# Optimization experiments

Measured on AMD Instinct MI355X. Metric: run time of the kernel, lower is better.

The kernel has to match this reference:

```python
import jax, jax.numpy as jnp
import numpy as np

HEADS = 12


def setup_inputs() -> dict:
    key = jax.random.key(0)
    ks = jax.random.split(key, 3)
    B, N, C = 4, 2048, 768
    x = jax.random.normal(ks[0], (B, N, C), dtype=jnp.float32)
    Wqkv = jax.random.normal(ks[1], (C, 3 * C), dtype=jnp.float32) * 0.02
    bqkv = jnp.zeros((3 * C,), dtype=jnp.float32)
    Wproj = jax.random.normal(ks[2], (C, C), dtype=jnp.float32) * 0.02
    bproj = jnp.zeros((C,), dtype=jnp.float32)
    return {"x": x, "Wqkv": Wqkv, "bqkv": bqkv, "Wproj": Wproj, "bproj": bproj}


def reference(x, Wqkv, bqkv, Wproj, bproj):
    B, N, C = x.shape
    h = HEADS
    d = C // h
    scale = d ** (-0.5)
    # QKV projection: (B, N, 3C) -> (3, B, h, N, d)
    qkv = (x @ Wqkv + bqkv).reshape(B, N, 3, h, d).transpose(2, 0, 3, 1, 4)
    q, k, v = qkv[0], qkv[1], qkv[2]
    # Full N x N attention scores per head (matches original explicit matmul)
    scores = jnp.einsum("bhnd,bhmd->bhnm", q, k) * scale
    attn = jax.nn.softmax(scores, axis=-1)
    out = jnp.einsum("bhnm,bhmd->bhnd", attn, v)  # (B, h, N, d)
    out = out.transpose(0, 2, 1, 3).reshape(B, N, C)
    return out @ Wproj + bproj
```

## Files before the change

kernel.cpp:

```cpp
#include <hip/hip_runtime.h>
#include <hip/hip_bf16.h>
#include <math.h>

#define B_ 4
#define N_ 2048
#define C_ 768
#define H_ 12
#define D_ 64
#define SC_LOG2E 0.18033688f

typedef __attribute__((ext_vector_type(8))) short bf16x8;
typedef __attribute__((ext_vector_type(4))) float f32x4;

#define MFMA16(A, B, C) __builtin_amdgcn_mfma_f32_16x16x32_bf16(A, B, C, 0, 0, 0)

#if __has_builtin(__builtin_amdgcn_exp2f)
#define EXP2F(x) __builtin_amdgcn_exp2f(x)
#else
#define EXP2F(x) exp2f(x)
#endif

__device__ __forceinline__ ushort f2bf(float f) {
    union { float f; unsigned u; } v; v.f = f;
    unsigned r = v.u + 0x7fffu + ((v.u >> 16) & 1u);
    return (ushort)(r >> 16);
}

#if __has_builtin(__builtin_amdgcn_cvt_pk_bf16_f32)
typedef __attribute__((ext_vector_type(2))) __bf16 bf16x2v;
__device__ __forceinline__ unsigned pack_bf2(float a, float b) {
    union { bf16x2v v; unsigned u; } cv;
    cv.v = __builtin_amdgcn_cvt_pk_bf16_f32(a, b);
    return cv.u;
}
#else
__device__ __forceinline__ unsigned pack_bf2(float a, float b) {
    union { __hip_bfloat162 h2; unsigned u; } cv;
    cv.h2 = __float22bfloat162_rn(make_float2(a, b));
    return cv.u;
}
#endif

__device__ __forceinline__ void gl_lds16(const ushort* g, ushort* l) {
    __builtin_amdgcn_global_load_lds(
        (const __attribute__((address_space(1))) unsigned*)g,
        (__attribute__((address_space(3))) unsigned*)l, 16, 0, 0);
}

__device__ __forceinline__ void tr_body(const float* __restrict__ W,
                                        ushort* __restrict__ Wt,
                                        int K, int N, int bx, int by, int t) {
    __shared__ float T[32][33];
    int k0 = by * 32, n0 = bx * 32;
    int r = t >> 3, c4 = (t & 7) * 4;
    float4 v = *(const float4*)&W[(size_t)(k0 + r) * N + n0 + c4];
    T[r][c4] = v.x; T[r][c4 + 1] = v.y; T[r][c4 + 2] = v.z; T[r][c4 + 3] = v.w;
    __syncthreads();
    union { ushort s[4]; unsigned long long u; } o;
    o.s[0] = f2bf(T[c4 + 0][r]);
    o.s[1] = f2bf(T[c4 + 1][r]);
    o.s[2] = f2bf(T[c4 + 2][r]);
    o.s[3] = f2bf(T[c4 + 3][r]);
    *(unsigned long long*)&Wt[(size_t)(n0 + r) * K + k0 + c4] = o.u;
}

__global__ __launch_bounds__(256) void prep(
    const float* __restrict__ x, ushort* __restrict__ xb,
    const float* __restrict__ Wqkv, ushort* __restrict__ Wqkvt,
    const float* __restrict__ Wproj, ushort* __restrict__ Wprojt)
{
    const int bid = blockIdx.x, t = threadIdx.x;
    if (bid < 3072) {
        int i = bid * 256 + t;
        const float4* p = (const float4*)x + 2 * (size_t)i;
        float4 a = p[0], bq = p[1];
        union { ushort s[8]; uint4 v; } u;
        u.s[0] = f2bf(a.x);  u.s[1] = f2bf(a.y);  u.s[2] = f2bf(a.z);  u.s[3] = f2bf(a.w);
        u.s[4] = f2bf(bq.x); u.s[5] = f2bf(bq.y); u.s[6] = f2bf(bq.z); u.s[7] = f2bf(bq.w);
        *(uint4*)&xb[(size_t)i * 8] = u.v;
    } else if (bid < 4800) {
        int id = bid - 3072;
        tr_body(Wqkv, Wqkvt, C_, 3 * C_, id % 72, id / 72, t);
    } else {
        int id = bid - 4800;
        tr_body(Wproj, Wprojt, C_, C_, id % 24, id / 24, t);
    }
}

__global__ __launch_bounds__(256) void vtrans(const ushort* __restrict__ qkvb,
                                              ushort* __restrict__ Vt) {
    __shared__ ushort T[64 * 64];
    const int tid = threadIdx.x;
    const int t0 = blockIdx.x * 64, bh = blockIdx.y;
    const int b = bh / H_, h = bh % H_;
#pragma unroll
    for (int i = 0; i < 2; i++) {
        int c = i * 256 + tid;
        int tok = c >> 3, dc = c & 7;
        uint4 v = *(const uint4*)&qkvb[((size_t)b * N_ + t0 + tok) * (3 * C_)
                                       + 2 * C_ + h * D_ + dc * 8];
        const ushort* vs = (const ushort*)&v;
#pragma unroll
        for (int j = 0; j < 8; j++) {
            int d = dc * 8 + j;
            int sc = (tok >> 3) ^ (d & 7) ^ (d >> 3);
            T[d * 64 + sc * 8 + (tok & 7)] = vs[j];
        }
    }
    __syncthreads();
#pragma unroll
    for (int i = 0; i < 2; i++) {
        int c = i * 256 + tid;
        int d = c >> 3, tc = c & 7;
        int sc = tc ^ (d & 7) ^ (d >> 3);
        uint4 o = *(const uint4*)&T[d * 64 + sc * 8];
        *(uint4*)&Vt[((size_t)bh * D_ + d) * N_ + t0 + tc * 8] = o;
    }
}

template <bool OBF>
__global__ __launch_bounds__(256) void gemm_bf16(
    const ushort* __restrict__ A, const ushort* __restrict__ Bt,
    const float* __restrict__ bias, void* __restrict__ outp,
    int M, int N, int K)
{
    __shared__ ushort Asl[128 * 64];
    __shared__ ushort Bsl[128 * 64];

    const int tid  = threadIdx.x;
    const int lane = tid & 63, w = tid >> 6;
    const int quad = lane >> 4, l16 = lane & 15;
    const int row0 = blockIdx.y * 128, col0 = blockIdx.x * 128;
    const int mh = (w >> 1) * 64, nh = (w & 1) * 64;

    f32x4 acc[4][4];
#pragma unroll
    for (int i = 0; i < 4; i++)
#pragma unroll
        for (int j = 0; j < 4; j++) acc[i][j] = (f32x4)0.f;

    for (int k0 = 0; k0 < K; k0 += 64) {
#pragma unroll
        for (int i = 0; i < 4; i++) {
            int c  = i * 256 + w * 64 + lane;
            int rr = c >> 3;
            int cc = (c & 7) ^ (rr & 7);
            int wb = (i * 256 + w * 64) * 8;
            gl_lds16(&A[(size_t)(row0 + rr) * K + k0 + cc * 8], &Asl[wb]);
            gl_lds16(&Bt[(size_t)(col0 + rr) * K + k0 + cc * 8], &Bsl[wb]);
        }
        __syncthreads();
#pragma unroll
        for (int h = 0; h < 2; h++) {
            const int sw = ((h * 4 + quad) ^ (l16 & 7)) * 8;
            bf16x8 af[4], bfr[4];
#pragma unroll
            for (int mt = 0; mt < 4; mt++)
                af[mt] = *(const bf16x8*)&Asl[(mh + mt * 16 + l16) * 64 + sw];
#pragma unroll
            for (int nt = 0; nt < 4; nt++)
                bfr[nt] = *(const bf16x8*)&Bsl[(nh + nt * 16 + l16) * 64 + sw];
#pragma unroll
            for (int mt = 0; mt < 4; mt++)
#pragma unroll
                for (int nt = 0; nt < 4; nt++)
                    acc[mt][nt] = MFMA16(af[mt], bfr[nt], acc[mt][nt]);
        }
        __syncthreads();
    }

    const float scl = (OBF && col0 < C_) ? SC_LOG2E : 1.f;
#pragma unroll
    for (int nt = 0; nt < 4; nt++) {
        int col = col0 + nh + nt * 16 + l16;
        float bv = bias[col];
#pragma unroll
        for (int mt = 0; mt < 4; mt++) {
            f32x4 v = acc[mt][nt];
#pragma unroll
            for (int r = 0; r < 4; r++) {
                int row = row0 + mh + mt * 16 + quad * 4 + r;
                if (OBF)
                    ((ushort*)outp)[(size_t)row * N + col] = f2bf((v[r] + bv) * scl);
                else
                    ((float*)outp)[(size_t)row * N + col] = v[r] + bv;
            }
        }
    }
}

__global__ __launch_bounds__(256) void attn_mfma(
    const ushort* __restrict__ qkvb, const ushort* __restrict__ Vt,
    ushort* __restrict__ attnb)
{
    __shared__ ushort Kd[3][64 * 64];
    __shared__ ushort Vd[3][64 * 64];
    __shared__ ushort Ptl[4 * 32 * 72];

    const int tid  = threadIdx.x;
    const int lane = tid & 63, w = tid >> 6;
    const int quad = lane >> 4, l16 = lane & 15;

    const int flat = blockIdx.y * 16 + blockIdx.x;
    const int nf   = (flat & 7) * 96 + (flat >> 3);
    const int bh   = nf >> 4, qt_ = nf & 15;
    const int b = bh / H_, h = bh % H_;
    const int q0 = qt_ * 128 + w * 32;
    const size_t rowbase = (size_t)b * N_;
    const int hoff = h * D_;
    ushort* Ptw = Ptl + w * 32 * 72;
    const f32x4 Z4 = {0.f, 0.f, 0.f, 0.f};

    const ushort* Kg = qkvb + rowbase * (3 * C_) + C_ + hoff;
    const ushort* Vg = Vt + (size_t)bh * D_ * N_;

    int rr0, cc0, rr1, cc1, wb0, wb1;
    {
        int c0 = w * 64 + lane, c1 = 256 + w * 64 + lane;
        rr0 = c0 >> 3; cc0 = (c0 & 7) ^ (rr0 & 7); wb0 = (w * 64) * 8;
        rr1 = c1 >> 3; cc1 = (c1 & 7) ^ (rr1 & 7); wb1 = (256 + w * 64) * 8;
    }
    const ushort* kp0 = Kg + (size_t)rr0 * (3 * C_) + cc0 * 8;
    const ushort* kp1 = Kg + (size_t)rr1 * (3 * C_) + cc1 * 8;
    const ushort* vp0 = Vg + (size_t)rr0 * N_ + cc0 * 8;
    const ushort* vp1 = Vg + (size_t)rr1 * N_ + cc1 * 8;

    bf16x8 Qf[2][2];
#pragma unroll
    for (int qt = 0; qt < 2; qt++)
#pragma unroll
        for (int c = 0; c < 2; c++)
            Qf[qt][c] = *(const bf16x8*)&qkvb[(rowbase + q0 + qt * 16 + l16) * (3 * C_)
                                              + hoff + c * 32 + quad * 8];

    f32x4 oacc[4][2];
#pragma unroll
    for (int dt = 0; dt < 4; dt++)
#pragma unroll
        for (int qt = 0; qt < 2; qt++) oacc[dt][qt] = (f32x4)0.f;
    float lrow[2] = {0.f, 0.f};

    const int NT = N_ / 64;
    gl_lds16(kp0, &Kd[0][wb0]); gl_lds16(vp0, &Vd[0][wb0]);
    gl_lds16(kp1, &Kd[0][wb1]); gl_lds16(vp1, &Vd[0][wb1]);
    kp0 += (size_t)64 * 3 * C_; kp1 += (size_t)64 * 3 * C_; vp0 += 64; vp1 += 64;
    gl_lds16(kp0, &Kd[1][wb0]); gl_lds16(vp0, &Vd[1][wb0]);
    gl_lds16(kp1, &Kd[1][wb1]); gl_lds16(vp1, &Vd[1][wb1]);
    kp0 += (size_t)64 * 3 * C_; kp1 += (size_t)64 * 3 * C_; vp0 += 64; vp1 += 64;
    asm volatile("s_waitcnt vmcnt(4)" ::: "memory");
    __builtin_amdgcn_s_barrier();
    __builtin_amdgcn_sched_barrier(0);

    int rd = 0;
    for (int t = 0; t < NT; ++t) {
        int wr = rd + 2; if (wr >= 3) wr -= 3;
        if (t + 2 < NT) {
            gl_lds16(kp0, &Kd[wr][wb0]); gl_lds16(vp0, &Vd[wr][wb0]);
            gl_lds16(kp1, &Kd[wr][wb1]); gl_lds16(vp1, &Vd[wr][wb1]);
            kp0 += (size_t)64 * 3 * C_; kp1 += (size_t)64 * 3 * C_;
            vp0 += 64; vp1 += 64;
        }
        __builtin_amdgcn_sched_barrier(0);

        const ushort* Kb = Kd[rd];
        const ushort* Vb = Vd[rd];

        f32x4 sacc[4][2];
        {
            bf16x8 kf[4];
#pragma unroll
            for (int kt = 0; kt < 4; kt++)
                kf[kt] = *(const bf16x8*)&Kb[(kt * 16 + l16) * 64
                                             + ((quad) ^ (l16 & 7)) * 8];
            __builtin_amdgcn_s_setprio(1);
#pragma unroll
            for (int kt = 0; kt < 4; kt++)
#pragma unroll
                for (int qt = 0; qt < 2; qt++)
                    sacc[kt][qt] = MFMA16(kf[kt], Qf[qt][0], Z4);
            __builtin_amdgcn_s_setprio(0);
        }
        {
            bf16x8 kf[4];
#pragma unroll
            for (int kt = 0; kt < 4; kt++)
                kf[kt] = *(const bf16x8*)&Kb[(kt * 16 + l16) * 64
                                             + ((4 | quad) ^ (l16 & 7)) * 8];
            __builtin_amdgcn_s_setprio(1);
#pragma unroll
            for (int kt = 0; kt < 4; kt++)
#pragma unroll
                for (int qt = 0; qt < 2; qt++)
                    sacc[kt][qt] = MFMA16(kf[kt], Qf[qt][1], sacc[kt][qt]);
            __builtin_amdgcn_s_setprio(0);
        }

#pragma unroll
        for (int qt = 0; qt < 2; qt++) {
            float sum = 0.f;
#pragma unroll
            for (int kt = 0; kt < 4; kt++) {
                float p0 = EXP2F(sacc[kt][qt][0]);
                float p1 = EXP2F(sacc[kt][qt][1]);
                float p2 = EXP2F(sacc[kt][qt][2]);
                float p3 = EXP2F(sacc[kt][qt][3]);
                sum += (p0 + p1) + (p2 + p3);
                uint2 pk;
                pk.x = pack_bf2(p0, p1);
                pk.y = pack_bf2(p2, p3);
                *(uint2*)&Ptw[(qt * 16 + l16) * 72 + kt * 16 + quad * 4] = pk;
            }
            lrow[qt] += sum;
        }

#pragma unroll
        for (int c = 0; c < 2; c++) {
            bf16x8 pf[2];
#pragma unroll
            for (int qt = 0; qt < 2; qt++)
                pf[qt] = *(const bf16x8*)&Ptw[(qt * 16 + l16) * 72
                                              + c * 32 + quad * 8];
            __builtin_amdgcn_s_setprio(1);
#pragma unroll
            for (int dt = 0; dt < 4; dt++) {
                bf16x8 vf = *(const bf16x8*)&Vb[(dt * 16 + l16) * 64
                                   + (((c << 2) | quad) ^ (l16 & 7)) * 8];
#pragma unroll
                for (int qt = 0; qt < 2; qt++)
                    oacc[dt][qt] = MFMA16(vf, pf[qt], oacc[dt][qt]);
            }
            __builtin_amdgcn_s_setprio(0);
        }

        if (t < NT - 2) asm volatile("s_waitcnt vmcnt(4)" ::: "memory");
        else            asm volatile("s_waitcnt vmcnt(0)" ::: "memory");
        __builtin_amdgcn_s_barrier();
        __builtin_amdgcn_sched_barrier(0);
        rd++; if (rd == 3) rd = 0;
    }

#pragma unroll
    for (int qt = 0; qt < 2; qt++) {
        float s = lrow[qt];
        s += __shfl_xor(s, 16, 64);
        s += __shfl_xor(s, 32, 64);
        float inv = 1.f / s;
        size_t orow = (rowbase + q0 + qt * 16 + l16) * C_ + hoff;
#pragma unroll
        for (int dt = 0; dt < 4; dt++) {
            union { ushort us[4]; unsigned long long u; } o;
#pragma unroll
            for (int r = 0; r < 4; r++) o.us[r] = f2bf(oacc[dt][qt][r] * inv);
            *(unsigned long long*)&attnb[orow + dt * 16 + quad * 4] = o.u;
        }
    }
}

extern "C" void kernel_launch(void* const* d_in, const int* in_sizes, int n_in,
                              void* d_out, int out_size, void* d_ws, size_t ws_size,
                              hipStream_t stream)
{
    const float* x     = (const float*)d_in[0];
    const float* Wqkv  = (const float*)d_in[1];
    const float* bqkv  = (const float*)d_in[2];
    const float* Wproj = (const float*)d_in[3];
    const float* bproj = (const float*)d_in[4];

    ushort* xb     = (ushort*)d_ws;
    ushort* Wqkvt  = xb + (size_t)B_ * N_ * C_;
    ushort* Wprojt = Wqkvt + (size_t)3 * C_ * C_;
    ushort* qkvb   = Wprojt + (size_t)C_ * C_;
    ushort* attnb  = qkvb + (size_t)B_ * N_ * 3 * C_;
    ushort* Vtb    = attnb + (size_t)B_ * N_ * C_;

    const int M = B_ * N_;

    prep<<<5376, 256, 0, stream>>>(x, xb, Wqkv, Wqkvt, Wproj, Wprojt);

    gemm_bf16<true><<<dim3((3 * C_) / 128, M / 128), 256, 0, stream>>>(
        xb, Wqkvt, bqkv, qkvb, M, 3 * C_, C_);

    vtrans<<<dim3(N_ / 64, B_ * H_), 256, 0, stream>>>(qkvb, Vtb);

    attn_mfma<<<dim3(N_ / 128, B_ * H_), 256, 0, stream>>>(qkvb, Vtb, attnb);

    gemm_bf16<false><<<dim3(C_ / 128, M / 128), 256, 0, stream>>>(
        attnb, Wprojt, bproj, d_out, M, C_, C_);
}
```

Before: 250.9 us.

## Fuse V transpose into QKV GEMM epilogue and use 8-wave attention blocks

The QKV GEMM epilogue now writes the V columns straight into the head-major transposed layout, so the separate vtrans kernel and its extra pass over V are gone. The attention kernel moves from 4 waves with 32 query rows each to 8 waves with 16 rows each. It also drops from triple to double buffering of K/V tiles with one load per thread, and sets launch bounds to 512 threads. This is meant to raise occupancy and cut register pressure. In exchange each K/V tile is reused across fewer query rows per wave, and a full vmcnt(0) wait every iteration reduces prefetch depth.

```diff
diff --git a/kernel.cpp b/kernel.cpp
--- a/kernel.cpp
+++ b/kernel.cpp
@@ -87,41 +87,11 @@
     }
 }
 
-__global__ __launch_bounds__(256) void vtrans(const ushort* __restrict__ qkvb,
-                                              ushort* __restrict__ Vt) {
-    __shared__ ushort T[64 * 64];
-    const int tid = threadIdx.x;
-    const int t0 = blockIdx.x * 64, bh = blockIdx.y;
-    const int b = bh / H_, h = bh % H_;
-#pragma unroll
-    for (int i = 0; i < 2; i++) {
-        int c = i * 256 + tid;
-        int tok = c >> 3, dc = c & 7;
-        uint4 v = *(const uint4*)&qkvb[((size_t)b * N_ + t0 + tok) * (3 * C_)
-                                       + 2 * C_ + h * D_ + dc * 8];
-        const ushort* vs = (const ushort*)&v;
-#pragma unroll
-        for (int j = 0; j < 8; j++) {
-            int d = dc * 8 + j;
-            int sc = (tok >> 3) ^ (d & 7) ^ (d >> 3);
-            T[d * 64 + sc * 8 + (tok & 7)] = vs[j];
-        }
-    }
-    __syncthreads();
-#pragma unroll
-    for (int i = 0; i < 2; i++) {
-        int c = i * 256 + tid;
-        int d = c >> 3, tc = c & 7;
-        int sc = tc ^ (d & 7) ^ (d >> 3);
-        uint4 o = *(const uint4*)&T[d * 64 + sc * 8];
-        *(uint4*)&Vt[((size_t)bh * D_ + d) * N_ + t0 + tc * 8] = o;
-    }
-}
-
 template <bool OBF>
 __global__ __launch_bounds__(256) void gemm_bf16(
     const ushort* __restrict__ A, const ushort* __restrict__ Bt,
     const float* __restrict__ bias, void* __restrict__ outp,
+    ushort* __restrict__ vtp,
     int M, int N, int K)
 {
     __shared__ ushort Asl[128 * 64];
@@ -169,33 +139,52 @@
         __syncthreads();
     }
 
-    const float scl = (OBF && col0 < C_) ? SC_LOG2E : 1.f;
-#pragma unroll
-    for (int nt = 0; nt < 4; nt++) {
-        int col = col0 + nh + nt * 16 + l16;
-        float bv = bias[col];
-#pragma unroll
-        for (int mt = 0; mt < 4; mt++) {
-            f32x4 v = acc[mt][nt];
-#pragma unroll
-            for (int r = 0; r < 4; r++) {
-                int row = row0 + mh + mt * 16 + quad * 4 + r;
-                if (OBF)
-                    ((ushort*)outp)[(size_t)row * N + col] = f2bf((v[r] + bv) * scl);
-                else
-                    ((float*)outp)[(size_t)row * N + col] = v[r] + bv;
+    if (OBF && col0 >= 2 * C_) {
+#pragma unroll
+        for (int nt = 0; nt < 4; nt++) {
+            int colh = col0 - 2 * C_ + nh + nt * 16 + l16;
+            int hh = colh >> 6, dd = colh & 63;
+            float bv = bias[col0 + nh + nt * 16 + l16];
+#pragma unroll
+            for (int mt = 0; mt < 4; mt++) {
+                f32x4 v = acc[mt][nt];
+                int row = row0 + mh + mt * 16 + quad * 4;
+                int bb = row >> 11, tok = row & (N_ - 1);
+                union { ushort us[4]; unsigned long long u; } o;
+#pragma unroll
+                for (int r = 0; r < 4; r++) o.us[r] = f2bf(v[r] + bv);
+                *(unsigned long long*)&vtp[((size_t)(bb * H_ + hh) * D_ + dd) * N_ + tok] = o.u;
             }
         }
-    }
-}
-
-__global__ __launch_bounds__(256) void attn_mfma(
+    } else {
+        const float scl = (OBF && col0 < C_) ? SC_LOG2E : 1.f;
+#pragma unroll
+        for (int nt = 0; nt < 4; nt++) {
+            int col = col0 + nh + nt * 16 + l16;
+            float bv = bias[col];
+#pragma unroll
+            for (int mt = 0; mt < 4; mt++) {
+                f32x4 v = acc[mt][nt];
+#pragma unroll
+                for (int r = 0; r < 4; r++) {
+                    int row = row0 + mh + mt * 16 + quad * 4 + r;
+                    if (OBF)
+                        ((ushort*)outp)[(size_t)row * N + col] = f2bf((v[r] + bv) * scl);
+                    else
+                        ((float*)outp)[(size_t)row * N + col] = v[r] + bv;
+                }
+            }
+        }
+    }
+}
+
+__global__ __launch_bounds__(512, 6) void attn_mfma(
     const ushort* __restrict__ qkvb, const ushort* __restrict__ Vt,
     ushort* __restrict__ attnb)
 {
-    __shared__ ushort Kd[3][64 * 64];
-    __shared__ ushort Vd[3][64 * 64];
-    __shared__ ushort Ptl[4 * 32 * 72];
+    __shared__ ushort Kd[2][64 * 64];
+    __shared__ ushort Vd[2][64 * 64];
+    __shared__ ushort Ptl[8 * 16 * 72];
 
     const int tid  = threadIdx.x;
     const int lane = tid & 63, w = tid >> 6;
@@ -205,67 +194,53 @@
     const int nf   = (flat & 7) * 96 + (flat >> 3);
     const int bh   = nf >> 4, qt_ = nf & 15;
     const int b = bh / H_, h = bh % H_;
-    const int q0 = qt_ * 128 + w * 32;
+    const int q0 = qt_ * 128 + w * 16;
     const size_t rowbase = (size_t)b * N_;
     const int hoff = h * D_;
-    ushort* Ptw = Ptl + w * 32 * 72;
+    ushort* Ptw = Ptl + w * 16 * 72;
     const f32x4 Z4 = {0.f, 0.f, 0.f, 0.f};
 
     const ushort* Kg = qkvb + rowbase * (3 * C_) + C_ + hoff;
     const ushort* Vg = Vt + (size_t)bh * D_ * N_;
 
-    int rr0, cc0, rr1, cc1, wb0, wb1;
-    {
-        int c0 = w * 64 + lane, c1 = 256 + w * 64 + lane;
-        rr0 = c0 >> 3; cc0 = (c0 & 7) ^ (rr0 & 7); wb0 = (w * 64) * 8;
-        rr1 = c1 >> 3; cc1 = (c1 & 7) ^ (rr1 & 7); wb1 = (256 + w * 64) * 8;
-    }
-    const ushort* kp0 = Kg + (size_t)rr0 * (3 * C_) + cc0 * 8;
-    const ushort* kp1 = Kg + (size_t)rr1 * (3 * C_) + cc1 * 8;
-    const ushort* vp0 = Vg + (size_t)rr0 * N_ + cc0 * 8;
-    const ushort* vp1 = Vg + (size_t)rr1 * N_ + cc1 * 8;
-
-    bf16x8 Qf[2][2];
-#pragma unroll
-    for (int qt = 0; qt < 2; qt++)
-#pragma unroll
-        for (int c = 0; c < 2; c++)
-            Qf[qt][c] = *(const bf16x8*)&qkvb[(rowbase + q0 + qt * 16 + l16) * (3 * C_)
-                                              + hoff + c * 32 + quad * 8];
-
-    f32x4 oacc[4][2];
-#pragma unroll
-    for (int dt = 0; dt < 4; dt++)
-#pragma unroll
-        for (int qt = 0; qt < 2; qt++) oacc[dt][qt] = (f32x4)0.f;
-    float lrow[2] = {0.f, 0.f};
+    const int rr = tid >> 3;
+    const int cc = (tid & 7) ^ (rr & 7);
+    const int wbase = w * 512;
+    const ushort* kp = Kg + (size_t)rr * (3 * C_) + cc * 8;
+    const ushort* vp = Vg + (size_t)rr * N_ + cc * 8;
+
+    bf16x8 Qf[2];
+#pragma unroll
+    for (int c = 0; c < 2; c++)
+        Qf[c] = *(const bf16x8*)&qkvb[(rowbase + q0 + l16) * (3 * C_)
+                                      + hoff + c * 32 + quad * 8];
+
+    f32x4 oacc[4];
+#pragma unroll
+    for (int dt = 0; dt < 4; dt++) oacc[dt] = (f32x4)0.f;
+    float lrow = 0.f;
 
     const int NT = N_ / 64;
-    gl_lds16(kp0, &Kd[0][wb0]); gl_lds16(vp0, &Vd[0][wb0]);
-    gl_lds16(kp1, &Kd[0][wb1]); gl_lds16(vp1, &Vd[0][wb1]);
-    kp0 += (size_t)64 * 3 * C_; kp1 += (size_t)64 * 3 * C_; vp0 += 64; vp1 += 64;
-    gl_lds16(kp0, &Kd[1][wb0]); gl_lds16(vp0, &Vd[1][wb0]);
-    gl_lds16(kp1, &Kd[1][wb1]); gl_lds16(vp1, &Vd[1][wb1]);
-    kp0 += (size_t)64 * 3 * C_; kp1 += (size_t)64 * 3 * C_; vp0 += 64; vp1 += 64;
-    asm volatile("s_waitcnt vmcnt(4)" ::: "memory");
+    gl_lds16(kp, &Kd[0][wbase]);
+    gl_lds16(vp, &Vd[0][wbase]);
+    kp += (size_t)64 * 3 * C_; vp += 64;
+    asm volatile("s_waitcnt vmcnt(0)" ::: "memory");
     __builtin_amdgcn_s_barrier();
     __builtin_amdgcn_sched_barrier(0);
 
-    int rd = 0;
     for (int t = 0; t < NT; ++t) {
-        int wr = rd + 2; if (wr >= 3) wr -= 3;
-        if (t + 2 < NT) {
-            gl_lds16(kp0, &Kd[wr][wb0]); gl_lds16(vp0, &Vd[wr][wb0]);
-            gl_lds16(kp1, &Kd[wr][wb1]); gl_lds16(vp1, &Vd[wr][wb1]);
-            kp0 += (size_t)64 * 3 * C_; kp1 += (size_t)64 * 3 * C_;
-            vp0 += 64; vp1 += 64;
+        const int rd = t & 1, wr = rd ^ 1;
+        if (t + 1 < NT) {
+            gl_lds16(kp, &Kd[wr][wbase]);
+            gl_lds16(vp, &Vd[wr][wbase]);
+            kp += (size_t)64 * 3 * C_; vp += 64;
         }
         __builtin_amdgcn_sched_barrier(0);
 
         const ushort* Kb = Kd[rd];
         const ushort* Vb = Vd[rd];
 
-        f32x4 sacc[4][2];
+        f32x4 sacc[4];
         {
             bf16x8 kf[4];
 #pragma unroll
@@ -275,9 +250,7 @@
             __builtin_amdgcn_s_setprio(1);
 #pragma unroll
             for (int kt = 0; kt < 4; kt++)
-#pragma unroll
-                for (int qt = 0; qt < 2; qt++)
-                    sacc[kt][qt] = MFMA16(kf[kt], Qf[qt][0], Z4);
+                sacc[kt] = MFMA16(kf[kt], Qf[0], Z4);
             __builtin_amdgcn_s_setprio(0);
         }
         {
@@ -289,68 +262,56 @@
             __builtin_amdgcn_s_setprio(1);
 #pragma unroll
             for (int kt = 0; kt < 4; kt++)
-#pragma unroll
-                for (int qt = 0; qt < 2; qt++)
-                    sacc[kt][qt] = MFMA16(kf[kt], Qf[qt][1], sacc[kt][qt]);
+                sacc[kt] = MFMA16(kf[kt], Qf[1], sacc[kt]);
             __builtin_amdgcn_s_setprio(0);
         }
 
-#pragma unroll
-        for (int qt = 0; qt < 2; qt++) {
+        {
             float sum = 0.f;
 #pragma unroll
             for (int kt = 0; kt < 4; kt++) {
-                float p0 = EXP2F(sacc[kt][qt][0]);
-                float p1 = EXP2F(sacc[kt][qt][1]);
-                float p2 = EXP2F(sacc[kt][qt][2]);
-                float p3 = EXP2F(sacc[kt][qt][3]);
+                float p0 = EXP2F(sacc[kt][0]);
+                float p1 = EXP2F(sacc[kt][1]);
+                float p2 = EXP2F(sacc[kt][2]);
+                float p3 = EXP2F(sacc[kt][3]);
                 sum += (p0 + p1) + (p2 + p3);
                 uint2 pk;
                 pk.x = pack_bf2(p0, p1);
                 pk.y = pack_bf2(p2, p3);
-                *(uint2*)&Ptw[(qt * 16 + l16) * 72 + kt * 16 + quad * 4] = pk;
+                *(uint2*)&Ptw[l16 * 72 + kt * 16 + quad * 4] = pk;
             }
-            lrow[qt] += sum;
+            lrow += sum;
         }
 
 #pragma unroll
         for (int c = 0; c < 2; c++) {
-            bf16x8 pf[2];
-#pragma unroll
-            for (int qt = 0; qt < 2; qt++)
-                pf[qt] = *(const bf16x8*)&Ptw[(qt * 16 + l16) * 72
-                                              + c * 32 + quad * 8];
+            bf16x8 pf = *(const bf16x8*)&Ptw[l16 * 72 + c * 32 + quad * 8];
             __builtin_amdgcn_s_setprio(1);
 #pragma unroll
             for (int dt = 0; dt < 4; dt++) {
                 bf16x8 vf = *(const bf16x8*)&Vb[(dt * 16 + l16) * 64
                                    + (((c << 2) | quad) ^ (l16 & 7)) * 8];
-#pragma unroll
-                for (int qt = 0; qt < 2; qt++)
-                    oacc[dt][qt] = MFMA16(vf, pf[qt], oacc[dt][qt]);
+                oacc[dt] = MFMA16(vf, pf, oacc[dt]);
             }
             __builtin_amdgcn_s_setprio(0);
         }
 
-        if (t < NT - 2) asm volatile("s_waitcnt vmcnt(4)" ::: "memory");
-        else            asm volatile("s_waitcnt vmcnt(0)" ::: "memory");
+        asm volatile("s_waitcnt vmcnt(0)" ::: "memory");
         __builtin_amdgcn_s_barrier();
         __builtin_amdgcn_sched_barrier(0);
-        rd++; if (rd == 3) rd = 0;
-    }
-
-#pragma unroll
-    for (int qt = 0; qt < 2; qt++) {
-        float s = lrow[qt];
+    }
+
+    {
+        float s = lrow;
         s += __shfl_xor(s, 16, 64);
         s += __shfl_xor(s, 32, 64);
         float inv = 1.f / s;
-        size_t orow = (rowbase + q0 + qt * 16 + l16) * C_ + hoff;
+        size_t orow = (rowbase + q0 + l16) * C_ + hoff;
 #pragma unroll
         for (int dt = 0; dt < 4; dt++) {
             union { ushort us[4]; unsigned long long u; } o;
 #pragma unroll
-            for (int r = 0; r < 4; r++) o.us[r] = f2bf(oacc[dt][qt][r] * inv);
+            for (int r = 0; r < 4; r++) o.us[r] = f2bf(oacc[dt][r] * inv);
             *(unsigned long long*)&attnb[orow + dt * 16 + quad * 4] = o.u;
         }
     }
@@ -378,12 +339,10 @@
     prep<<<5376, 256, 0, stream>>>(x, xb, Wqkv, Wqkvt, Wproj, Wprojt);
 
     gemm_bf16<true><<<dim3((3 * C_) / 128, M / 128), 256, 0, stream>>>(
-        xb, Wqkvt, bqkv, qkvb, M, 3 * C_, C_);
-
-    vtrans<<<dim3(N_ / 64, B_ * H_), 256, 0, stream>>>(qkvb, Vtb);
-
-    attn_mfma<<<dim3(N_ / 128, B_ * H_), 256, 0, stream>>>(qkvb, Vtb, attnb);
+        xb, Wqkvt, bqkv, qkvb, Vtb, M, 3 * C_, C_);
+
+    attn_mfma<<<dim3(N_ / 128, B_ * H_), 512, 0, stream>>>(qkvb, Vtb, attnb);
 
     gemm_bf16<false><<<dim3(C_ / 128, M / 128), 256, 0, stream>>>(
-        attnb, Wprojt, bproj, d_out, M, C_, C_);
-}
+        attnb, Wprojt, bproj, d_out, nullptr, M, C_, C_);
+}
```

Result: faster. 225.4 us (-10.2%).

## Fuse V transpose into QKV GEMM epilogue and double-buffer attention K/V

Applied to the files above, without the earlier changes.

The QKV GEMM epilogue now writes the V columns straight into the head-major transposed Vt layout, packing four consecutive tokens per 8-byte store. This removes the separate vtrans kernel launch and its read and write of V. The attention kernel also drops from a triple-buffered to a double-buffered K/V pipeline with full vmcnt(0) waits each iteration. That cuts LDS use, which may allow more blocks per CU, but it reduces how far loads run ahead of compute and so exposes more load latency.

```diff
diff --git a/kernel.cpp b/kernel.cpp
--- a/kernel.cpp
+++ b/kernel.cpp
@@ -87,41 +87,11 @@
     }
 }
 
-__global__ __launch_bounds__(256) void vtrans(const ushort* __restrict__ qkvb,
-                                              ushort* __restrict__ Vt) {
-    __shared__ ushort T[64 * 64];
-    const int tid = threadIdx.x;
-    const int t0 = blockIdx.x * 64, bh = blockIdx.y;
-    const int b = bh / H_, h = bh % H_;
-#pragma unroll
-    for (int i = 0; i < 2; i++) {
-        int c = i * 256 + tid;
-        int tok = c >> 3, dc = c & 7;
-        uint4 v = *(const uint4*)&qkvb[((size_t)b * N_ + t0 + tok) * (3 * C_)
-                                       + 2 * C_ + h * D_ + dc * 8];
-        const ushort* vs = (const ushort*)&v;
-#pragma unroll
-        for (int j = 0; j < 8; j++) {
-            int d = dc * 8 + j;
-            int sc = (tok >> 3) ^ (d & 7) ^ (d >> 3);
-            T[d * 64 + sc * 8 + (tok & 7)] = vs[j];
-        }
-    }
-    __syncthreads();
-#pragma unroll
-    for (int i = 0; i < 2; i++) {
-        int c = i * 256 + tid;
-        int d = c >> 3, tc = c & 7;
-        int sc = tc ^ (d & 7) ^ (d >> 3);
-        uint4 o = *(const uint4*)&T[d * 64 + sc * 8];
-        *(uint4*)&Vt[((size_t)bh * D_ + d) * N_ + t0 + tc * 8] = o;
-    }
-}
-
 template <bool OBF>
 __global__ __launch_bounds__(256) void gemm_bf16(
     const ushort* __restrict__ A, const ushort* __restrict__ Bt,
     const float* __restrict__ bias, void* __restrict__ outp,
+    ushort* __restrict__ vtp,
     int M, int N, int K)
 {
     __shared__ ushort Asl[128 * 64];
@@ -169,21 +139,40 @@
         __syncthreads();
     }
 
-    const float scl = (OBF && col0 < C_) ? SC_LOG2E : 1.f;
-#pragma unroll
-    for (int nt = 0; nt < 4; nt++) {
-        int col = col0 + nh + nt * 16 + l16;
-        float bv = bias[col];
-#pragma unroll
-        for (int mt = 0; mt < 4; mt++) {
-            f32x4 v = acc[mt][nt];
-#pragma unroll
-            for (int r = 0; r < 4; r++) {
-                int row = row0 + mh + mt * 16 + quad * 4 + r;
-                if (OBF)
-                    ((ushort*)outp)[(size_t)row * N + col] = f2bf((v[r] + bv) * scl);
-                else
-                    ((float*)outp)[(size_t)row * N + col] = v[r] + bv;
+    if (OBF && col0 >= 2 * C_) {
+#pragma unroll
+        for (int nt = 0; nt < 4; nt++) {
+            int colh = col0 - 2 * C_ + nh + nt * 16 + l16;
+            int hh = colh >> 6, dd = colh & 63;
+            float bv = bias[col0 + nh + nt * 16 + l16];
+#pragma unroll
+            for (int mt = 0; mt < 4; mt++) {
+                f32x4 v = acc[mt][nt];
+                int row = row0 + mh + mt * 16 + quad * 4;
+                int bb = row >> 11, tok = row & (N_ - 1);
+                union { ushort us[4]; unsigned long long u; } o;
+#pragma unroll
+                for (int r = 0; r < 4; r++) o.us[r] = f2bf(v[r] + bv);
+                *(unsigned long long*)&vtp[((size_t)(bb * H_ + hh) * D_ + dd) * N_ + tok] = o.u;
+            }
+        }
+    } else {
+        const float scl = (OBF && col0 < C_) ? SC_LOG2E : 1.f;
+#pragma unroll
+        for (int nt = 0; nt < 4; nt++) {
+            int col = col0 + nh + nt * 16 + l16;
+            float bv = bias[col];
+#pragma unroll
+            for (int mt = 0; mt < 4; mt++) {
+                f32x4 v = acc[mt][nt];
+#pragma unroll
+                for (int r = 0; r < 4; r++) {
+                    int row = row0 + mh + mt * 16 + quad * 4 + r;
+                    if (OBF)
+                        ((ushort*)outp)[(size_t)row * N + col] = f2bf((v[r] + bv) * scl);
+                    else
+                        ((float*)outp)[(size_t)row * N + col] = v[r] + bv;
+                }
             }
         }
     }
@@ -193,8 +182,8 @@
     const ushort* __restrict__ qkvb, const ushort* __restrict__ Vt,
     ushort* __restrict__ attnb)
 {
-    __shared__ ushort Kd[3][64 * 64];
-    __shared__ ushort Vd[3][64 * 64];
+    __shared__ ushort Kd[2][64 * 64];
+    __shared__ ushort Vd[2][64 * 64];
     __shared__ ushort Ptl[4 * 32 * 72];
 
     const int tid  = threadIdx.x;
@@ -244,17 +233,13 @@
     gl_lds16(kp0, &Kd[0][wb0]); gl_lds16(vp0, &Vd[0][wb0]);
     gl_lds16(kp1, &Kd[0][wb1]); gl_lds16(vp1, &Vd[0][wb1]);
     kp0 += (size_t)64 * 3 * C_; kp1 += (size_t)64 * 3 * C_; vp0 += 64; vp1 += 64;
-    gl_lds16(kp0, &Kd[1][wb0]); gl_lds16(vp0, &Vd[1][wb0]);
-    gl_lds16(kp1, &Kd[1][wb1]); gl_lds16(vp1, &Vd[1][wb1]);
-    kp0 += (size_t)64 * 3 * C_; kp1 += (size_t)64 * 3 * C_; vp0 += 64; vp1 += 64;
-    asm volatile("s_waitcnt vmcnt(4)" ::: "memory");
+    asm volatile("s_waitcnt vmcnt(0)" ::: "memory");
     __builtin_amdgcn_s_barrier();
     __builtin_amdgcn_sched_barrier(0);
 
-    int rd = 0;
     for (int t = 0; t < NT; ++t) {
-        int wr = rd + 2; if (wr >= 3) wr -= 3;
-        if (t + 2 < NT) {
+        const int rd = t & 1, wr = rd ^ 1;
+        if (t + 1 < NT) {
             gl_lds16(kp0, &Kd[wr][wb0]); gl_lds16(vp0, &Vd[wr][wb0]);
             gl_lds16(kp1, &Kd[wr][wb1]); gl_lds16(vp1, &Vd[wr][wb1]);
             kp0 += (size_t)64 * 3 * C_; kp1 += (size_t)64 * 3 * C_;
@@ -332,11 +317,9 @@
             __builtin_amdgcn_s_setprio(0);
         }
 
-        if (t < NT - 2) asm volatile("s_waitcnt vmcnt(4)" ::: "memory");
-        else            asm volatile("s_waitcnt vmcnt(0)" ::: "memory");
+        asm volatile("s_waitcnt vmcnt(0)" ::: "memory");
         __builtin_amdgcn_s_barrier();
         __builtin_amdgcn_sched_barrier(0);
-        rd++; if (rd == 3) rd = 0;
     }
 
 #pragma unroll
@@ -378,12 +361,10 @@
     prep<<<5376, 256, 0, stream>>>(x, xb, Wqkv, Wqkvt, Wproj, Wprojt);
 
     gemm_bf16<true><<<dim3((3 * C_) / 128, M / 128), 256, 0, stream>>>(
-        xb, Wqkvt, bqkv, qkvb, M, 3 * C_, C_);
-
-    vtrans<<<dim3(N_ / 64, B_ * H_), 256, 0, stream>>>(qkvb, Vtb);
+        xb, Wqkvt, bqkv, qkvb, Vtb, M, 3 * C_, C_);
 
     attn_mfma<<<dim3(N_ / 128, B_ * H_), 256, 0, stream>>>(qkvb, Vtb, attnb);
 
     gemm_bf16<false><<<dim3(C_ / 128, M / 128), 256, 0, stream>>>(
-        attnb, Wprojt, bproj, d_out, M, C_, C_);
-}
+        attnb, Wprojt, bproj, d_out, nullptr, M, C_, C_);
+}
```

New measurement: 232.2 us. -7.4%, faster.
